# Kernel tuning notes

Hardware: AMD Instinct MI355X
Metric: run time of the kernel (lower is better)

## Reference

```python
import jax, jax.numpy as jnp
import numpy as np

N_RET, N_ORIG, N_EDGE = 200000, 100000, 800000
D_FEAT, HIDDEN, OUT = 128, 128, 64


def _gcn(x_src, ridx, cidx, n_src, n_dst, W, b):
    # GCNConv (add_self_loops=False), bipartite symmetric normalization:
    # norm_e = deg_src[row]^-1/2 * deg_dst[col]^-1/2
    h = x_src @ W                                            # [n_src, H]
    ones = jnp.ones(ridx.shape[0], h.dtype)
    deg_s = jax.ops.segment_sum(ones, ridx, num_segments=n_src)
    deg_d = jax.ops.segment_sum(ones, cidx, num_segments=n_dst)
    inv_s = jnp.where(deg_s > 0, jax.lax.rsqrt(jnp.maximum(deg_s, 1.0)), 0.0)
    inv_d = jnp.where(deg_d > 0, jax.lax.rsqrt(jnp.maximum(deg_d, 1.0)), 0.0)
    norm = inv_s[ridx] * inv_d[cidx]                         # [E]
    out = jax.ops.segment_sum(h[ridx] * norm[:, None], cidx, num_segments=n_dst)
    return out + b


def _sage(x_src, x_dst, sidx, didx, n_dst, Wl, bl, Wr):
    # SAGEConv: mean-aggregate raw src features, then lin_l(agg)+bias + lin_r(x_dst)
    deg = jax.ops.segment_sum(jnp.ones(sidx.shape[0], x_src.dtype), didx, num_segments=n_dst)
    agg = jax.ops.segment_sum(x_src[sidx], didx, num_segments=n_dst)
    agg = agg / jnp.maximum(deg, 1.0)[:, None]
    return agg @ Wl + bl + x_dst @ Wr


def setup_inputs() -> dict:
    key = jax.random.key(0)
    ks = jax.random.split(key, 20)
    def w(k, fan_in, shape):
        return jax.random.normal(k, shape, jnp.float32) / np.sqrt(fan_in)
    inp = {
        "x_ret": jax.random.normal(ks[0], (N_RET, D_FEAT), jnp.float32),
        "x_orig": jax.random.normal(ks[1], (N_ORIG, D_FEAT), jnp.float32),
        "ret_idx": jax.random.randint(ks[2], (N_EDGE,), 0, N_RET, jnp.int32),
        "orig_idx": jax.random.randint(ks[3], (N_EDGE,), 0, N_ORIG, jnp.int32),
        # layer 1 (lazy in = D_FEAT)
        "W_g1": w(ks[4], D_FEAT, (D_FEAT, HIDDEN)), "b_g1": jnp.zeros((HIDDEN,), jnp.float32),
        "Wl1": w(ks[5], D_FEAT, (D_FEAT, HIDDEN)), "bl1": jnp.zeros((HIDDEN,), jnp.float32),
        "Wr1": w(ks[6], D_FEAT, (D_FEAT, HIDDEN)),
        # layer 2 (in = HIDDEN)
        "W_g2": w(ks[7], HIDDEN, (HIDDEN, HIDDEN)), "b_g2": jnp.zeros((HIDDEN,), jnp.float32),
        "Wl2": w(ks[8], HIDDEN, (HIDDEN, HIDDEN)), "bl2": jnp.zeros((HIDDEN,), jnp.float32),
        "Wr2": w(ks[9], HIDDEN, (HIDDEN, HIDDEN)),
        # final linear
        "W_out": w(ks[10], HIDDEN, (HIDDEN, OUT)), "b_out": jnp.zeros((OUT,), jnp.float32),
    }
    return inp


def reference(x_ret, x_orig, ret_idx, orig_idx,
              W_g1, b_g1, Wl1, bl1, Wr1,
              W_g2, b_g2, Wl2, bl2, Wr2,
              W_out, b_out):
    # layer 1: HeteroConv over two relations, then relu per node type
    o1 = jax.nn.relu(_gcn(x_ret, ret_idx, orig_idx, N_RET, N_ORIG, W_g1, b_g1))
    r1 = jax.nn.relu(_sage(x_orig, x_ret, orig_idx, ret_idx, N_RET, Wl1, bl1, Wr1))
    # layer 2
    o2 = jax.nn.relu(_gcn(r1, ret_idx, orig_idx, N_RET, N_ORIG, W_g2, b_g2))
    r2 = jax.nn.relu(_sage(o1, r1, orig_idx, ret_idx, N_RET, Wl2, bl2, Wr2))
    # final linear readout (original code indexes x_dict['author'], which is absent
    # after HeteroConv; we read out the 'original_tweet' node type)
    return o2 @ W_out + b_out
```

## Files before the change

kernel.cpp:

```cpp
#include <hip/hip_runtime.h>

#define N_RET  200000
#define N_ORIG 100000
#define N_EDGE 800000
#define NB_RET  ((N_RET  + 511) >> 9)
#define NB_ORIG ((N_ORIG + 511) >> 9)
#define NBIN    ((N_EDGE + 8191) / 8192)
#define NBLK_HO ((N_ORIG + 63) / 64)
#define NBLK_XR ((N_RET + 63) / 64)

typedef __attribute__((ext_vector_type(8))) short bf16x8;
typedef __attribute__((ext_vector_type(4))) float f32x4;

__device__ __forceinline__ ushort f2bf(float f) {
    union { float f; unsigned u; } v; v.f = f;
    unsigned r = v.u + 0x7FFFu + ((v.u >> 16) & 1u);
    return (ushort)(r >> 16);
}
__device__ __forceinline__ float bf2f(ushort u) {
    union { unsigned u; float f; } v; v.u = ((unsigned)u) << 16;
    return v.f;
}
__device__ __forceinline__ int swz(int byteoff) {
    return byteoff ^ ((byteoff >> 4) & 0x70);
}

__global__ void prep_kernel(const float* __restrict__ Wl1, const float* __restrict__ Wr1,
                            const float* __restrict__ Wg2, const float* __restrict__ Wout,
                            ushort* __restrict__ wtl1, ushort* __restrict__ wtr1,
                            ushort* __restrict__ wtg2, ushort* __restrict__ wto,
                            int* __restrict__ bcnt) {
    const int b = blockIdx.x, t = threadIdx.x;
    if (b == 224) {
        for (int i = t; i < 1024; i += 256) bcnt[i] = 0;
        return;
    }
    const float* W; ushort* WT; int base, nshift;
    if (b < 64)       { W = Wl1;  WT = wtl1; base = b;       nshift = 7; }
    else if (b < 128) { W = Wr1;  WT = wtr1; base = b - 64;  nshift = 7; }
    else if (b < 192) { W = Wg2;  WT = wtg2; base = b - 128; nshift = 7; }
    else              { W = Wout; WT = wto;  base = b - 192; nshift = 6; }
    int i = base * 256 + t;
    int k = i >> nshift, n = i & ((1 << nshift) - 1);
    WT[n * 128 + k] = f2bf(W[i]);
}

__global__ __launch_bounds__(256) void bucket_count(const int* __restrict__ ridx,
                                                    const int* __restrict__ cidx,
                                                    int* __restrict__ bcnt1,
                                                    int* __restrict__ bcnt2) {
    __shared__ int h1[512], h2[512];
    const int t = threadIdx.x;
    const int c0 = blockIdx.x * 8192;
    for (int i = t; i < 512; i += 256) { h1[i] = 0; h2[i] = 0; }
    __syncthreads();
    for (int i = t; i < 8192; i += 256) {
        int e = c0 + i;
        if (e < N_EDGE) {
            atomicAdd(&h1[ridx[e] >> 9], 1);
            atomicAdd(&h2[cidx[e] >> 9], 1);
        }
    }
    __syncthreads();
    for (int b = t; b < NB_RET; b += 256)
        if (h1[b]) atomicAdd(&bcnt1[b], h1[b]);
    for (int b = t; b < NB_ORIG; b += 256)
        if (h2[b]) atomicAdd(&bcnt2[b], h2[b]);
}

__global__ __launch_bounds__(256) void scan_buckets(const int* __restrict__ bcnt1,
                                                    int* __restrict__ boff1, int* __restrict__ bcur1,
                                                    const int* __restrict__ bcnt2,
                                                    int* __restrict__ boff2, int* __restrict__ bcur2,
                                                    int* __restrict__ off_ret,
                                                    int* __restrict__ off_orig) {
    __shared__ int sm[256];
    const int t = threadIdx.x;
    {
        int a0 = (2 * t     < NB_RET) ? bcnt1[2 * t]     : 0;
        int a1 = (2 * t + 1 < NB_RET) ? bcnt1[2 * t + 1] : 0;
        sm[t] = a0 + a1;
        __syncthreads();
        for (int d = 1; d < 256; d <<= 1) {
            int v = (t >= d) ? sm[t - d] : 0;
            __syncthreads(); sm[t] += v; __syncthreads();
        }
        int tb = t ? sm[t - 1] : 0;
        if (2 * t < NB_RET)     { boff1[2 * t]     = tb;      bcur1[2 * t]     = tb; }
        if (2 * t + 1 < NB_RET) { boff1[2 * t + 1] = tb + a0; bcur1[2 * t + 1] = tb + a0; }
        if (t == 0) { boff1[NB_RET] = N_EDGE; off_ret[N_RET] = N_EDGE; }
        __syncthreads();
    }
    {
        int a0 = (2 * t     < NB_ORIG) ? bcnt2[2 * t]     : 0;
        int a1 = (2 * t + 1 < NB_ORIG) ? bcnt2[2 * t + 1] : 0;
        sm[t] = a0 + a1;
        __syncthreads();
        for (int d = 1; d < 256; d <<= 1) {
            int v = (t >= d) ? sm[t - d] : 0;
            __syncthreads(); sm[t] += v; __syncthreads();
        }
        int tb = t ? sm[t - 1] : 0;
        if (2 * t < NB_ORIG)     { boff2[2 * t]     = tb;      bcur2[2 * t]     = tb; }
        if (2 * t + 1 < NB_ORIG) { boff2[2 * t + 1] = tb + a0; bcur2[2 * t + 1] = tb + a0; }
        if (t == 0) { boff2[NB_ORIG] = N_EDGE; off_orig[N_ORIG] = N_EDGE; }
    }
}

__global__ __launch_bounds__(256) void bin_both(const int* __restrict__ ridx,
                                                const int* __restrict__ cidx,
                                                int* __restrict__ bcur1, int* __restrict__ bcur2,
                                                int* __restrict__ binned1, int* __restrict__ binned2) {
    __shared__ int hist[512], base[512], lcur[512];
    const int t = threadIdx.x;
    const bool second = blockIdx.x >= NBIN;
    const int* dst = second ? cidx : ridx;
    const int* src = second ? ridx : cidx;
    int* bcur = second ? bcur2 : bcur1;
    int* binned = second ? binned2 : binned1;
    const int nbuckets = second ? NB_ORIG : NB_RET;
    const int c0 = (second ? blockIdx.x - NBIN : blockIdx.x) * 8192;
    for (int i = t; i < 512; i += 256) { hist[i] = 0; lcur[i] = 0; }
    __syncthreads();
    for (int i = t; i < 8192; i += 256) {
        int e = c0 + i;
        if (e < N_EDGE) atomicAdd(&hist[dst[e] >> 9], 1);
    }
    __syncthreads();
    for (int b = t; b < nbuckets; b += 256)
        base[b] = hist[b] > 0 ? atomicAdd(&bcur[b], hist[b]) : 0;
    __syncthreads();
    for (int i = t; i < 8192; i += 256) {
        int e = c0 + i;
        if (e < N_EDGE) {
            int d = dst[e];
            int b = d >> 9;
            int r = atomicAdd(&lcur[b], 1);
            binned[base[b] + r] = ((d & 511) << 18) | src[e];
        }
    }
}

__global__ __launch_bounds__(256) void fill_both(const int* __restrict__ binned1,
                                                 const int* __restrict__ boff1,
                                                 int* __restrict__ off_ret, int* __restrict__ el1,
                                                 const int* __restrict__ binned2,
                                                 const int* __restrict__ boff2,
                                                 int* __restrict__ off_orig, int* __restrict__ el2) {
    __shared__ int hist[512];
    __shared__ int sm[256];
    const int t = threadIdx.x;
    const bool second = blockIdx.x >= NB_RET;
    const int bkt = second ? blockIdx.x - NB_RET : blockIdx.x;
    const int* binned = second ? binned2 : binned1;
    const int* boff = second ? boff2 : boff1;
    int* off = second ? off_orig : off_ret;
    int* el  = second ? el2 : el1;
    const int nnodes = second ? N_ORIG : N_RET;
    const int base = bkt << 9;
    const int nvalid = min(512, nnodes - base);
    const int s0 = boff[bkt], s1 = boff[bkt + 1];
    for (int i = t; i < 512; i += 256) hist[i] = 0;
    __syncthreads();
    for (int i = s0 + t; i < s1; i += 256)
        atomicAdd(&hist[binned[i] >> 18], 1);
    __syncthreads();
    int a0 = hist[2 * t], a1 = hist[2 * t + 1];
    sm[t] = a0 + a1;
    __syncthreads();
    for (int d = 1; d < 256; d <<= 1) {
        int v = (t >= d) ? sm[t - d] : 0;
        __syncthreads(); sm[t] += v; __syncthreads();
    }
    int tb = (t ? sm[t - 1] : 0) + s0;
    if (2 * t < nvalid)     off[base + 2 * t]     = tb;
    if (2 * t + 1 < nvalid) off[base + 2 * t + 1] = tb + a0;
    hist[2 * t] = tb;
    hist[2 * t + 1] = tb + a0;
    __syncthreads();
    for (int i = s0 + t; i < s1; i += 256) {
        int v = binned[i];
        int p = atomicAdd(&hist[v >> 18], 1);
        el[p] = v & 0x3FFFF;
    }
}

__global__ __launch_bounds__(256) void gemm_lin(const float* __restrict__ Ao,
                                                const float* __restrict__ Ar,
                                                const ushort* __restrict__ WTl,
                                                const ushort* __restrict__ WTr,
                                                ushort* __restrict__ hoB,
                                                ushort* __restrict__ xrB) {
    __shared__ ushort Wlds[128 * 128];
    const int t = threadIdx.x;
    const bool second = blockIdx.x >= NBLK_HO;
    const float* A = second ? Ar : Ao;
    const ushort* WT = second ? WTr : WTl;
    ushort* outp = second ? xrB : hoB;
    const int M = second ? N_RET : N_ORIG;
    const int i0 = (second ? blockIdx.x - NBLK_HO : blockIdx.x) * 64;

    #pragma unroll
    for (int it = 0; it < 8; ++it) {
        int idx = t + 256 * it;
        int n = idx >> 4, u = idx & 15;
        *(bf16x8*)&Wlds[swz(n * 256 + u * 16) >> 1] = *(const bf16x8*)&WT[idx * 8];
    }

    const int w = t >> 6, l = t & 63;
    const int r16 = l & 15, kg = l >> 4;
    const int arow = min(i0 + 16 * w + r16, M - 1);

    bf16x8 a[4];
    #pragma unroll
    for (int ks = 0; ks < 4; ++ks) {
        const float* p = &A[(size_t)arow * 128 + ks * 32 + kg * 8];
        float4 v0 = *(const float4*)p;
        float4 v1 = *(const float4*)(p + 4);
        bf16x8 f;
        f[0] = (short)f2bf(v0.x); f[1] = (short)f2bf(v0.y);
        f[2] = (short)f2bf(v0.z); f[3] = (short)f2bf(v0.w);
        f[4] = (short)f2bf(v1.x); f[5] = (short)f2bf(v1.y);
        f[6] = (short)f2bf(v1.z); f[7] = (short)f2bf(v1.w);
        a[ks] = f;
    }
    __syncthreads();

    f32x4 acc[8];
    #pragma unroll
    for (int cf = 0; cf < 8; ++cf) acc[cf] = (f32x4){0.f, 0.f, 0.f, 0.f};
    #pragma unroll
    for (int cf = 0; cf < 8; ++cf) {
        int n = cf * 16 + r16;
        #pragma unroll
        for (int ks = 0; ks < 4; ++ks) {
            bf16x8 b = *(const bf16x8*)&Wlds[swz(n * 256 + kg * 16 + ks * 64) >> 1];
            acc[cf] = __builtin_amdgcn_mfma_f32_16x16x32_bf16(a[ks], b, acc[cf], 0, 0, 0);
        }
    }
    #pragma unroll
    for (int r = 0; r < 4; ++r) {
        int gr = i0 + 16 * w + 4 * kg + r;
        if (gr >= M) continue;
        #pragma unroll
        for (int cf = 0; cf < 8; ++cf)
            outp[(size_t)gr * 128 + cf * 16 + r16] = f2bf(acc[cf][r]);
    }
}

__global__ void gather_sage(const ushort* __restrict__ ho, const ushort* __restrict__ xr,
                            const int* __restrict__ off, const int* __restrict__ slist,
                            const float* __restrict__ bl, ushort* __restrict__ r1s) {
    int gt = blockIdx.x * 256 + threadIdx.x;
    int node = gt >> 4;
    if (node >= N_RET) return;
    int o8 = gt & 15;
    int s = off[node], e = off[node + 1];
    float acc[8] = {0.f, 0.f, 0.f, 0.f, 0.f, 0.f, 0.f, 0.f};
    for (int i = s; i < e; ++i) {
        int sn = slist[i];
        bf16x8 v = *(const bf16x8*)&ho[(size_t)sn * 128 + o8 * 8];
        #pragma unroll
        for (int j = 0; j < 8; ++j) acc[j] += bf2f((ushort)v[j]);
    }
    int deg = e - s;
    float rinv = 1.0f / fmaxf((float)deg, 1.0f);
    float sinv = deg > 0 ? rsqrtf((float)deg) : 0.f;
    bf16x8 xv = *(const bf16x8*)&xr[(size_t)node * 128 + o8 * 8];
    bf16x8 ov;
    #pragma unroll
    for (int j = 0; j < 8; ++j) {
        float v = fmaxf(acc[j] * rinv + bf2f((ushort)xv[j]) + bl[o8 * 8 + j], 0.f) * sinv;
        ov[j] = (short)f2bf(v);
    }
    *(bf16x8*)&r1s[(size_t)node * 128 + o8 * 8] = ov;
}

__global__ void gather_sum(const ushort* __restrict__ src,
                           const int* __restrict__ off, const int* __restrict__ slist,
                           ushort* __restrict__ dst) {
    int gt = blockIdx.x * 256 + threadIdx.x;
    int node = gt >> 4;
    if (node >= N_ORIG) return;
    int o8 = gt & 15;
    int s = off[node], e = off[node + 1];
    float acc[8] = {0.f, 0.f, 0.f, 0.f, 0.f, 0.f, 0.f, 0.f};
    for (int i = s; i < e; ++i) {
        int sn = slist[i];
        bf16x8 v = *(const bf16x8*)&src[(size_t)sn * 128 + o8 * 8];
        #pragma unroll
        for (int j = 0; j < 8; ++j) acc[j] += bf2f((ushort)v[j]);
    }
    bf16x8 ov;
    #pragma unroll
    for (int j = 0; j < 8; ++j) ov[j] = (short)f2bf(acc[j]);
    *(bf16x8*)&dst[(size_t)node * 128 + o8 * 8] = ov;
}

__global__ __launch_bounds__(256) void gemm_t_out(
    const ushort* __restrict__ g, const ushort* __restrict__ WTg,
    const ushort* __restrict__ WTo, const int* __restrict__ off,
    const float* __restrict__ bg, const float* __restrict__ bo,
    float* __restrict__ out, int M) {
    __shared__ ushort Alds[64 * 128];
    __shared__ ushort Wlds[128 * 128];
    const int t = threadIdx.x;
    const int i0 = blockIdx.x * 64;

    #pragma unroll
    for (int it = 0; it < 8; ++it) {
        int idx = t + 256 * it;
        int n = idx >> 4, u = idx & 15;
        *(bf16x8*)&Wlds[swz(n * 256 + u * 16) >> 1] = *(const bf16x8*)&WTg[idx * 8];
    }
    #pragma unroll
    for (int it = 0; it < 4; ++it) {
        int idx = t + 256 * it;
        int row = idx >> 4, u = idx & 15;
        int gr = min(i0 + row, M - 1);
        bf16x8 v = *(const bf16x8*)&g[(size_t)gr * 128 + u * 8];
        *(bf16x8*)&Alds[swz(row * 256 + u * 16) >> 1] = v;
    }
    __syncthreads();

    const int w = t >> 6, l = t & 63;
    const int r16 = l & 15, kg = l >> 4;
    const int arow = 16 * w + r16;

    bf16x8 a[4];
    #pragma unroll
    for (int ks = 0; ks < 4; ++ks)
        a[ks] = *(const bf16x8*)&Alds[swz(arow * 256 + kg * 16 + ks * 64) >> 1];
    f32x4 acc[8];
    #pragma unroll
    for (int cf = 0; cf < 8; ++cf) acc[cf] = (f32x4){0.f, 0.f, 0.f, 0.f};
    #pragma unroll
    for (int cf = 0; cf < 8; ++cf) {
        int n = cf * 16 + r16;
        #pragma unroll
        for (int ks = 0; ks < 4; ++ks) {
            bf16x8 b = *(const bf16x8*)&Wlds[swz(n * 256 + kg * 16 + ks * 64) >> 1];
            acc[cf] = __builtin_amdgcn_mfma_f32_16x16x32_bf16(a[ks], b, acc[cf], 0, 0, 0);
        }
    }
    __syncthreads();

    #pragma unroll
    for (int r = 0; r < 4; ++r) {
        int row = 16 * w + 4 * kg + r;
        int grc = min(i0 + row, M - 1);
        int dg = off[grc + 1] - off[grc];
        float di = dg > 0 ? rsqrtf((float)dg) : 0.f;
        #pragma unroll
        for (int cf = 0; cf < 8; ++cf) {
            int col = cf * 16 + r16;
            float v = fmaxf(acc[cf][r] * di + bg[col], 0.f);
            Alds[swz(row * 256 + col * 2) >> 1] = f2bf(v);
        }
    }
    #pragma unroll
    for (int it = 0; it < 4; ++it) {
        int idx = t + 256 * it;
        int n = idx >> 4, u = idx & 15;
        *(bf16x8*)&Wlds[swz(n * 256 + u * 16) >> 1] = *(const bf16x8*)&WTo[idx * 8];
    }
    __syncthreads();

    bf16x8 a2[4];
    #pragma unroll
    for (int ks = 0; ks < 4; ++ks)
        a2[ks] = *(const bf16x8*)&Alds[swz(arow * 256 + kg * 16 + ks * 64) >> 1];
    f32x4 acc2[4];
    #pragma unroll
    for (int cf = 0; cf < 4; ++cf) acc2[cf] = (f32x4){0.f, 0.f, 0.f, 0.f};
    #pragma unroll
    for (int cf = 0; cf < 4; ++cf) {
        int n = cf * 16 + r16;
        #pragma unroll
        for (int ks = 0; ks < 4; ++ks) {
            bf16x8 b = *(const bf16x8*)&Wlds[swz(n * 256 + kg * 16 + ks * 64) >> 1];
            acc2[cf] = __builtin_amdgcn_mfma_f32_16x16x32_bf16(a2[ks], b, acc2[cf], 0, 0, 0);
        }
    }
    #pragma unroll
    for (int r = 0; r < 4; ++r) {
        int gr = i0 + 16 * w + 4 * kg + r;
        if (gr >= M) continue;
        #pragma unroll
        for (int cf = 0; cf < 4; ++cf) {
            int col = cf * 16 + r16;
            out[(size_t)gr * 64 + col] = acc2[cf][r] + bo[col];
        }
    }
}

extern "C" void kernel_launch(void* const* d_in, const int* in_sizes, int n_in,
                              void* d_out, int out_size, void* d_ws, size_t ws_size,
                              hipStream_t stream) {
    const float* x_ret    = (const float*)d_in[0];
    const float* x_orig   = (const float*)d_in[1];
    const int*   ret_idx  = (const int*)d_in[2];
    const int*   orig_idx = (const int*)d_in[3];
    const float* Wl1  = (const float*)d_in[6];
    const float* bl1  = (const float*)d_in[7];
    const float* Wr1  = (const float*)d_in[8];
    const float* Wg2  = (const float*)d_in[9];
    const float* bg2  = (const float*)d_in[10];
    const float* Wout = (const float*)d_in[14];
    const float* bout = (const float*)d_in[15];
    float* out = (float*)d_out;

    ushort* hoB  = (ushort*)d_ws;
    ushort* xrB  = hoB + (size_t)N_ORIG * 128;
    ushort* r1sB = xrB + (size_t)N_RET * 128;
    ushort* wtl1 = r1sB + (size_t)N_RET * 128;
    ushort* wtr1 = wtl1 + 16384;
    ushort* wtg2 = wtr1 + 16384;
    ushort* wto  = wtg2 + 16384;
    int* off_ret  = (int*)(wto + 8192);
    int* off_orig = off_ret + N_RET + 1;
    int* bcnt1    = off_orig + N_ORIG + 1;
    int* bcnt2    = bcnt1 + 512;
    int* boff1    = bcnt2 + 512;
    int* boff2    = boff1 + 512;
    int* bcur1    = boff2 + 512;
    int* bcur2    = bcur1 + 512;
    int* el1      = bcur2 + 512;
    int* el2      = el1 + N_EDGE;
    int* binned1  = el2 + N_EDGE;
    int* binned2  = binned1 + N_EDGE;

    prep_kernel<<<225, 256, 0, stream>>>(Wl1, Wr1, Wg2, Wout, wtl1, wtr1, wtg2, wto, bcnt1);

    bucket_count<<<NBIN, 256, 0, stream>>>(ret_idx, orig_idx, bcnt1, bcnt2);
    scan_buckets<<<1, 256, 0, stream>>>(bcnt1, boff1, bcur1, bcnt2, boff2, bcur2,
                                        off_ret, off_orig);
    bin_both<<<2 * NBIN, 256, 0, stream>>>(ret_idx, orig_idx, bcur1, bcur2, binned1, binned2);
    fill_both<<<NB_RET + NB_ORIG, 256, 0, stream>>>(binned1, boff1, off_ret, el1,
                                                    binned2, boff2, off_orig, el2);

    gemm_lin<<<NBLK_HO + NBLK_XR, 256, 0, stream>>>(
        x_orig, x_ret, wtl1, wtr1, hoB, xrB);

    gather_sage<<<(N_RET * 16) / 256, 256, 0, stream>>>(hoB, xrB, off_ret, el1, bl1, r1sB);

    gather_sum<<<(N_ORIG * 16) / 256, 256, 0, stream>>>(r1sB, off_orig, el2, hoB);

    gemm_t_out<<<(N_ORIG + 63) / 64, 256, 0, stream>>>(hoB, wtg2, wto, off_orig,
                                                       bg2, bout, out, N_ORIG);
}
```

Baseline: 247.7 us.

## Shrink edge chunks for binning and double rows per block in gemm_lin

Edge chunks for bucket_count and bin_both shrink from 8192 to 2048 edges, so the binning kernels launch about four times as many blocks and use more of the GPU. The gemm_lin kernel now handles 128 rows per block in two 64-row sub-tiles that share each LDS weight fragment. This halves the number of per-block loads of the 32 KB weight tile and gives the MFMAs more independent work to interleave. In exchange it raises register pressure and adds more global atomics on the bucket cursors.

```diff
diff --git a/kernel.cpp b/kernel.cpp
--- a/kernel.cpp
+++ b/kernel.cpp
@@ -5,9 +5,10 @@
 #define N_EDGE 800000
 #define NB_RET  ((N_RET  + 511) >> 9)
 #define NB_ORIG ((N_ORIG + 511) >> 9)
-#define NBIN    ((N_EDGE + 8191) / 8192)
-#define NBLK_HO ((N_ORIG + 63) / 64)
-#define NBLK_XR ((N_RET + 63) / 64)
+#define ECHUNK  2048
+#define NCHUNK  ((N_EDGE + ECHUNK - 1) / ECHUNK)
+#define NBLK_HO ((N_ORIG + 127) / 128)
+#define NBLK_XR ((N_RET + 127) / 128)
 
 typedef __attribute__((ext_vector_type(8))) short bf16x8;
 typedef __attribute__((ext_vector_type(4))) float f32x4;
@@ -51,10 +52,10 @@
                                                     int* __restrict__ bcnt2) {
     __shared__ int h1[512], h2[512];
     const int t = threadIdx.x;
-    const int c0 = blockIdx.x * 8192;
+    const int c0 = blockIdx.x * ECHUNK;
     for (int i = t; i < 512; i += 256) { h1[i] = 0; h2[i] = 0; }
     __syncthreads();
-    for (int i = t; i < 8192; i += 256) {
+    for (int i = t; i < ECHUNK; i += 256) {
         int e = c0 + i;
         if (e < N_EDGE) {
             atomicAdd(&h1[ridx[e] >> 9], 1);
@@ -113,16 +114,16 @@
                                                 int* __restrict__ binned1, int* __restrict__ binned2) {
     __shared__ int hist[512], base[512], lcur[512];
     const int t = threadIdx.x;
-    const bool second = blockIdx.x >= NBIN;
+    const bool second = blockIdx.x >= NCHUNK;
     const int* dst = second ? cidx : ridx;
     const int* src = second ? ridx : cidx;
     int* bcur = second ? bcur2 : bcur1;
     int* binned = second ? binned2 : binned1;
     const int nbuckets = second ? NB_ORIG : NB_RET;
-    const int c0 = (second ? blockIdx.x - NBIN : blockIdx.x) * 8192;
+    const int c0 = (second ? blockIdx.x - NCHUNK : blockIdx.x) * ECHUNK;
     for (int i = t; i < 512; i += 256) { hist[i] = 0; lcur[i] = 0; }
     __syncthreads();
-    for (int i = t; i < 8192; i += 256) {
+    for (int i = t; i < ECHUNK; i += 256) {
         int e = c0 + i;
         if (e < N_EDGE) atomicAdd(&hist[dst[e] >> 9], 1);
     }
@@ -130,7 +131,7 @@
     for (int b = t; b < nbuckets; b += 256)
         base[b] = hist[b] > 0 ? atomicAdd(&bcur[b], hist[b]) : 0;
     __syncthreads();
-    for (int i = t; i < 8192; i += 256) {
+    for (int i = t; i < ECHUNK; i += 256) {
         int e = c0 + i;
         if (e < N_EDGE) {
             int d = dst[e];
@@ -198,7 +199,7 @@
     const ushort* WT = second ? WTr : WTl;
     ushort* outp = second ? xrB : hoB;
     const int M = second ? N_RET : N_ORIG;
-    const int i0 = (second ? blockIdx.x - NBLK_HO : blockIdx.x) * 64;
+    const int i0 = (second ? blockIdx.x - NBLK_HO : blockIdx.x) * 128;
 
     #pragma unroll
     for (int it = 0; it < 8; ++it) {
@@ -209,43 +210,51 @@
 
     const int w = t >> 6, l = t & 63;
     const int r16 = l & 15, kg = l >> 4;
-    const int arow = min(i0 + 16 * w + r16, M - 1);
-
-    bf16x8 a[4];
-    #pragma unroll
-    for (int ks = 0; ks < 4; ++ks) {
-        const float* p = &A[(size_t)arow * 128 + ks * 32 + kg * 8];
-        float4 v0 = *(const float4*)p;
-        float4 v1 = *(const float4*)(p + 4);
-        bf16x8 f;
-        f[0] = (short)f2bf(v0.x); f[1] = (short)f2bf(v0.y);
-        f[2] = (short)f2bf(v0.z); f[3] = (short)f2bf(v0.w);
-        f[4] = (short)f2bf(v1.x); f[5] = (short)f2bf(v1.y);
-        f[6] = (short)f2bf(v1.z); f[7] = (short)f2bf(v1.w);
-        a[ks] = f;
-    }
-    __syncthreads();
-
-    f32x4 acc[8];
-    #pragma unroll
-    for (int cf = 0; cf < 8; ++cf) acc[cf] = (f32x4){0.f, 0.f, 0.f, 0.f};
+
+    bf16x8 a[2][4];
+    #pragma unroll
+    for (int s = 0; s < 2; ++s) {
+        int arow = min(i0 + s * 64 + 16 * w + r16, M - 1);
+        #pragma unroll
+        for (int ks = 0; ks < 4; ++ks) {
+            const float* p = &A[(size_t)arow * 128 + ks * 32 + kg * 8];
+            float4 v0 = *(const float4*)p;
+            float4 v1 = *(const float4*)(p + 4);
+            bf16x8 f;
+            f[0] = (short)f2bf(v0.x); f[1] = (short)f2bf(v0.y);
+            f[2] = (short)f2bf(v0.z); f[3] = (short)f2bf(v0.w);
+            f[4] = (short)f2bf(v1.x); f[5] = (short)f2bf(v1.y);
+            f[6] = (short)f2bf(v1.z); f[7] = (short)f2bf(v1.w);
+            a[s][ks] = f;
+        }
+    }
+    __syncthreads();
+
+    f32x4 acc[2][8];
+    #pragma unroll
+    for (int s = 0; s < 2; ++s)
+        #pragma unroll
+        for (int cf = 0; cf < 8; ++cf) acc[s][cf] = (f32x4){0.f, 0.f, 0.f, 0.f};
     #pragma unroll
     for (int cf = 0; cf < 8; ++cf) {
         int n = cf * 16 + r16;
         #pragma unroll
         for (int ks = 0; ks < 4; ++ks) {
             bf16x8 b = *(const bf16x8*)&Wlds[swz(n * 256 + kg * 16 + ks * 64) >> 1];
-            acc[cf] = __builtin_amdgcn_mfma_f32_16x16x32_bf16(a[ks], b, acc[cf], 0, 0, 0);
-        }
-    }
-    #pragma unroll
-    for (int r = 0; r < 4; ++r) {
-        int gr = i0 + 16 * w + 4 * kg + r;
-        if (gr >= M) continue;
-        #pragma unroll
-        for (int cf = 0; cf < 8; ++cf)
-            outp[(size_t)gr * 128 + cf * 16 + r16] = f2bf(acc[cf][r]);
-    }
+            acc[0][cf] = __builtin_amdgcn_mfma_f32_16x16x32_bf16(a[0][ks], b, acc[0][cf], 0, 0, 0);
+            acc[1][cf] = __builtin_amdgcn_mfma_f32_16x16x32_bf16(a[1][ks], b, acc[1][cf], 0, 0, 0);
+        }
+    }
+    #pragma unroll
+    for (int s = 0; s < 2; ++s)
+        #pragma unroll
+        for (int r = 0; r < 4; ++r) {
+            int gr = i0 + s * 64 + 16 * w + 4 * kg + r;
+            if (gr >= M) continue;
+            #pragma unroll
+            for (int cf = 0; cf < 8; ++cf)
+                outp[(size_t)gr * 128 + cf * 16 + r16] = f2bf(acc[s][cf][r]);
+        }
 }
 
 __global__ void gather_sage(const ushort* __restrict__ ho, const ushort* __restrict__ xr,
@@ -432,10 +441,10 @@
 
     prep_kernel<<<225, 256, 0, stream>>>(Wl1, Wr1, Wg2, Wout, wtl1, wtr1, wtg2, wto, bcnt1);
 
-    bucket_count<<<NBIN, 256, 0, stream>>>(ret_idx, orig_idx, bcnt1, bcnt2);
+    bucket_count<<<NCHUNK, 256, 0, stream>>>(ret_idx, orig_idx, bcnt1, bcnt2);
     scan_buckets<<<1, 256, 0, stream>>>(bcnt1, boff1, bcur1, bcnt2, boff2, bcur2,
                                         off_ret, off_orig);
-    bin_both<<<2 * NBIN, 256, 0, stream>>>(ret_idx, orig_idx, bcur1, bcur2, binned1, binned2);
+    bin_both<<<2 * NCHUNK, 256, 0, stream>>>(ret_idx, orig_idx, bcur1, bcur2, binned1, binned2);
     fill_both<<<NB_RET + NB_ORIG, 256, 0, stream>>>(binned1, boff1, off_ret, el1,
                                                     binned2, boff2, off_orig, el2);
 
```

After: 231.3 us. 1.07x faster.
